# Kernel tuning notes

Measured on AMD Instinct MI355X. Metric: run time of the kernel, lower is better.

The kernel has to match this reference:

```python
import jax, jax.numpy as jnp
import numpy as np

LN_EPS = 1e-5


def setup_inputs() -> dict:
    key = jax.random.key(0)
    ks = jax.random.split(key, 6)
    B, I, H = 16384, 512, 512
    x = jax.random.normal(ks[0], (B, I), dtype=jnp.float32)
    h_prev = jax.random.normal(ks[1], (B, H), dtype=jnp.float32)
    c_prev = jax.random.normal(ks[2], (B, H), dtype=jnp.float32)
    # packed gate weights in i|f|g|o order (equivalent to 8 separate matmuls)
    W_i = jax.random.normal(ks[3], (I, 4 * H), dtype=jnp.float32) * (1.0 / np.sqrt(I))
    W_h = jax.random.normal(ks[4], (H, 4 * H), dtype=jnp.float32) * (1.0 / np.sqrt(H))
    # biases: b_i=0, b_f=1, b_g=0, b_o=0 as in the torch module
    b = jnp.concatenate([jnp.zeros(H), jnp.ones(H), jnp.zeros(H), jnp.zeros(H)]).astype(jnp.float32)
    ln_weight = jnp.ones((H,), dtype=jnp.float32)
    ln_bias = jnp.zeros((H,), dtype=jnp.float32)
    return {"x": x, "h_prev": h_prev, "c_prev": c_prev, "W_i": W_i, "W_h": W_h,
            "b": b, "ln_weight": ln_weight, "ln_bias": ln_bias}


def layer_norm(h, w, bias):
    mu = jnp.mean(h, axis=-1, keepdims=True)
    var = jnp.var(h, axis=-1, keepdims=True)
    return (h - mu) * jax.lax.rsqrt(var + LN_EPS) * w + bias


def reference(x, h_prev, c_prev, W_i, W_h, b, ln_weight, ln_bias):
    H = h_prev.shape[-1]
    # two fused GEMMs covering all 4 gates: [B, 4H]
    gates = x @ W_i + h_prev @ W_h + b
    i, f, g, o = jnp.split(gates, 4, axis=-1)
    i = jax.nn.sigmoid(i)
    f = jax.nn.sigmoid(f)
    g = jnp.tanh(g)
    o = jax.nn.sigmoid(o)
    c = f * c_prev + i * g
    h = o * jnp.tanh(c)
    h = layer_norm(h, ln_weight, ln_bias)
    return (h, c)
```

## Files before the change

### kernel.cpp

```cpp
#include <hip/hip_runtime.h>
#include <cstdint>
#include <cstddef>

typedef unsigned short ushort_t;
typedef __attribute__((ext_vector_type(8))) short bf16x8;
typedef __attribute__((ext_vector_type(4))) float f32x4;

#define MROWS 16384
#define KDIM  1024
#define NDIM  2048
#define HDIM  512

static __device__ __forceinline__ unsigned short f2bf(float f) {
    unsigned int u = __float_as_uint(f);
    u += 0x7fffu + ((u >> 16) & 1u);
    return (unsigned short)(u >> 16);
}

static __device__ __forceinline__ float sigmoid_f(float x) {
    return 1.0f / (1.0f + __expf(-x));
}
static __device__ __forceinline__ float tanh_f(float x) {
    float t = __expf(2.0f * x);
    return 1.0f - 2.0f / (t + 1.0f);
}

__global__ __launch_bounds__(256) void pack_ab(const float* __restrict__ x,
                                               const float* __restrict__ hp,
                                               const float* __restrict__ Wi,
                                               const float* __restrict__ Wh,
                                               ushort_t* __restrict__ A,
                                               ushort_t* __restrict__ Bt) {
    __shared__ ushort_t sm[64][72];
    const int tid = threadIdx.x;
    if (blockIdx.x < 8192) {
        int t = blockIdx.x * 256 + tid;
        int row = t >> 7;
        int kc = (t & 127) << 3;
        const float* src = (kc < 512) ? (x + (size_t)row * 512 + kc)
                                      : (hp + (size_t)row * 512 + (kc - 512));
        float4 v0 = ((const float4*)src)[0];
        float4 v1 = ((const float4*)src)[1];
        ushort_t o[8] __attribute__((aligned(16)));
        o[0] = f2bf(v0.x); o[1] = f2bf(v0.y); o[2] = f2bf(v0.z); o[3] = f2bf(v0.w);
        o[4] = f2bf(v1.x); o[5] = f2bf(v1.y); o[6] = f2bf(v1.z); o[7] = f2bf(v1.w);
        *((uint4*)(A + (size_t)row * KDIM + kc)) = *((const uint4*)o);
    } else {
        int b2 = blockIdx.x - 8192;
        int kt = b2 >> 5;
        int ct = b2 & 31;
        const float* W = (kt < 8) ? (Wi + (size_t)(kt * 64) * NDIM)
                                  : (Wh + (size_t)((kt - 8) * 64) * NDIM);
        int c0 = (tid & 15) * 4;
        int r0 = tid >> 4;
#pragma unroll
        for (int r = 0; r < 4; ++r) {
            int krow = r * 16 + r0;
            float4 v = *((const float4*)(W + (size_t)krow * NDIM + ct * 64 + c0));
            sm[krow][c0 + 0] = f2bf(v.x);
            sm[krow][c0 + 1] = f2bf(v.y);
            sm[krow][c0 + 2] = f2bf(v.z);
            sm[krow][c0 + 3] = f2bf(v.w);
        }
        __syncthreads();
        int g = (ct * 64) >> 9;
        int h0 = ct * 64 - g * 512;
#pragma unroll
        for (int q = tid; q < 512; q += 256) {
            int cc = q >> 3;
            int kc = (q & 7) * 8;
            ushort_t o[8] __attribute__((aligned(16)));
#pragma unroll
            for (int j = 0; j < 8; ++j) o[j] = sm[kc + j][cc];
            int np = 4 * (h0 + cc) + g;
            *((uint4*)(Bt + (size_t)np * KDIM + kt * 64 + kc)) = *((const uint4*)o);
        }
    }
}

__global__ __launch_bounds__(256, 4) void gemm_cell(const ushort_t* __restrict__ A,
                                                    const ushort_t* __restrict__ Bt,
                                                    const float* __restrict__ b,
                                                    const float* __restrict__ c_prev,
                                                    float* __restrict__ h_out,
                                                    float* __restrict__ c_out) {
    __shared__ float smem_f[10240];
    ushort_t* Als = (ushort_t*)smem_f;
    ushort_t* Bls = Als + 256 * 64;

    const int tid  = threadIdx.x;
    const int w    = tid >> 6;
    const int lane = tid & 63;
    int bid = blockIdx.x;
    int lid = (bid >> 3) + (bid & 7) * 256;
    const int m0 = (lid >> 5) * 256;
    const int n0 = (lid & 31) * 64;
    const int wm = w * 64;
    const int lr   = lane & 15;
    const int quad = lane >> 4;
    const int sw   = lr & 7;

    f32x4 zero = {0.f, 0.f, 0.f, 0.f};
    f32x4 acc[4][4];
#pragma unroll
    for (int i = 0; i < 4; ++i)
#pragma unroll
        for (int j = 0; j < 4; ++j) acc[i][j] = zero;

    for (int kt = 0; kt < KDIM / 64; ++kt) {
#pragma unroll
        for (int r = 0; r < 8; ++r) {
            int c = r * 256 + tid;
            int trow = c >> 3;
            int chg = (c & 7) ^ (trow & 7);
            const ushort_t* ga = A + (size_t)(m0 + trow) * KDIM + kt * 64 + chg * 8;
            __builtin_amdgcn_global_load_lds(
                (const __attribute__((address_space(1))) void*)ga,
                (__attribute__((address_space(3))) void*)((char*)Als + c * 16),
                16, 0, 0);
        }
#pragma unroll
        for (int r = 0; r < 2; ++r) {
            int c = r * 256 + tid;
            int trow = c >> 3;
            int chg = (c & 7) ^ (trow & 7);
            const ushort_t* gb = Bt + (size_t)(n0 + trow) * KDIM + kt * 64 + chg * 8;
            __builtin_amdgcn_global_load_lds(
                (const __attribute__((address_space(1))) void*)gb,
                (__attribute__((address_space(3))) void*)((char*)Bls + c * 16),
                16, 0, 0);
        }
        __syncthreads();

#pragma unroll
        for (int kk = 0; kk < 2; ++kk) {
            bf16x8 af[4], bfr[4];
            int ch = kk * 4 + quad;
#pragma unroll
            for (int t2 = 0; t2 < 4; ++t2) {
                int ra = wm + t2 * 16 + lr;
                af[t2] = *((const bf16x8*)(Als + (ra * 8 + (ch ^ sw)) * 8));
            }
#pragma unroll
            for (int t2 = 0; t2 < 4; ++t2) {
                int rb = t2 * 16 + lr;
                bfr[t2] = *((const bf16x8*)(Bls + (rb * 8 + (ch ^ sw)) * 8));
            }
#pragma unroll
            for (int tm = 0; tm < 4; ++tm)
#pragma unroll
                for (int tn = 0; tn < 4; ++tn)
                    acc[tm][tn] = __builtin_amdgcn_mfma_f32_16x16x32_bf16(
                        af[tm], bfr[tn], acc[tm][tn], 0, 0, 0);
        }
        __syncthreads();
    }

    float* scr = smem_f + w * 1024;
    const int rr = lane >> 2;
    const int hg0 = (n0 >> 2) + (lane & 3) * 4;
    const float4 bi4 = *((const float4*)(b + hg0));
    const float4 bff = *((const float4*)(b + 512 + hg0));
    const float4 bgg = *((const float4*)(b + 1024 + hg0));
    const float4 boo = *((const float4*)(b + 1536 + hg0));
    const float bi[4] = {bi4.x, bi4.y, bi4.z, bi4.w};
    const float bfv[4] = {bff.x, bff.y, bff.z, bff.w};
    const float bg[4] = {bgg.x, bgg.y, bgg.z, bgg.w};
    const float bo[4] = {boo.x, boo.y, boo.z, boo.w};

#pragma unroll
    for (int tm = 0; tm < 4; ++tm) {
#pragma unroll
        for (int tn = 0; tn < 4; ++tn) {
            int c = tn * 16 + lr;
#pragma unroll
            for (int rg = 0; rg < 4; ++rg) {
                int r = quad * 4 + rg;
                int blk = (c >> 2) ^ r;
                scr[r * 64 + blk * 4 + (c & 3)] = acc[tm][tn][rg];
            }
        }
        float4 gv[4];
#pragma unroll
        for (int j = 0; j < 4; ++j) {
            int cb = (lane & 3) * 4 + j;
            gv[j] = *((const float4*)(scr + rr * 64 + (cb ^ rr) * 4));
        }
        int grow = m0 + wm + tm * 16 + rr;
        float4 cp4 = *((const float4*)(c_prev + (size_t)grow * HDIM + hg0));
        const float cpv[4] = {cp4.x, cp4.y, cp4.z, cp4.w};
        float cn[4], hv[4];
#pragma unroll
        for (int j = 0; j < 4; ++j) {
            float iv = sigmoid_f(gv[j].x + bi[j]);
            float fv = sigmoid_f(gv[j].y + bfv[j]);
            float g2 = tanh_f(gv[j].z + bg[j]);
            float ov = sigmoid_f(gv[j].w + bo[j]);
            cn[j] = fv * cpv[j] + iv * g2;
            hv[j] = ov * tanh_f(cn[j]);
        }
        float4 cno = {cn[0], cn[1], cn[2], cn[3]};
        float4 hvo = {hv[0], hv[1], hv[2], hv[3]};
        *((float4*)(c_out + (size_t)grow * HDIM + hg0)) = cno;
        *((float4*)(h_out + (size_t)grow * HDIM + hg0)) = hvo;
    }
}

__global__ __launch_bounds__(256) void ln_kernel(float* __restrict__ h,
                                                 const float* __restrict__ lw,
                                                 const float* __restrict__ lb) {
    int w = threadIdx.x >> 6;
    int lane = threadIdx.x & 63;
    int row = blockIdx.x * 4 + w;
    float* p = h + (size_t)row * HDIM + lane * 8;
    float4 a = ((const float4*)p)[0];
    float4 c = ((const float4*)p)[1];
    float s  = a.x + a.y + a.z + a.w + c.x + c.y + c.z + c.w;
    float ss = a.x * a.x + a.y * a.y + a.z * a.z + a.w * a.w +
               c.x * c.x + c.y * c.y + c.z * c.z + c.w * c.w;
#pragma unroll
    for (int off = 32; off > 0; off >>= 1) {
        s  += __shfl_xor(s, off);
        ss += __shfl_xor(ss, off);
    }
    float mu = s * (1.0f / 512.0f);
    float var = ss * (1.0f / 512.0f) - mu * mu;
    float rstd = rsqrtf(var + 1e-5f);
    const float* wp = lw + lane * 8;
    const float* bp = lb + lane * 8;
    float4 w0 = ((const float4*)wp)[0];
    float4 w1 = ((const float4*)wp)[1];
    float4 b0 = ((const float4*)bp)[0];
    float4 b1 = ((const float4*)bp)[1];
    a.x = (a.x - mu) * rstd * w0.x + b0.x;
    a.y = (a.y - mu) * rstd * w0.y + b0.y;
    a.z = (a.z - mu) * rstd * w0.z + b0.z;
    a.w = (a.w - mu) * rstd * w0.w + b0.w;
    c.x = (c.x - mu) * rstd * w1.x + b1.x;
    c.y = (c.y - mu) * rstd * w1.y + b1.y;
    c.z = (c.z - mu) * rstd * w1.z + b1.z;
    c.w = (c.w - mu) * rstd * w1.w + b1.w;
    ((float4*)p)[0] = a;
    ((float4*)p)[1] = c;
}

extern "C" void kernel_launch(void* const* d_in, const int* in_sizes, int n_in,
                              void* d_out, int out_size, void* d_ws, size_t ws_size,
                              hipStream_t stream) {
    const float* x      = (const float*)d_in[0];
    const float* h_prev = (const float*)d_in[1];
    const float* c_prev = (const float*)d_in[2];
    const float* W_i    = (const float*)d_in[3];
    const float* W_h    = (const float*)d_in[4];
    const float* b      = (const float*)d_in[5];
    const float* ln_w   = (const float*)d_in[6];
    const float* ln_b   = (const float*)d_in[7];

    float* h_out = (float*)d_out;
    float* c_out = h_out + (size_t)MROWS * HDIM;

    ushort_t* A  = (ushort_t*)d_ws;
    ushort_t* Bt = A + (size_t)MROWS * KDIM;

    pack_ab<<<8192 + 512, 256, 0, stream>>>(x, h_prev, W_i, W_h, A, Bt);
    gemm_cell<<<2048, 256, 0, stream>>>(A, Bt, b, c_prev, h_out, c_out);
    ln_kernel<<<MROWS / 4, 256, 0, stream>>>(h_out, ln_w, ln_b);
}
```

Baseline: 254.8 us.

## Pre-pack A and B into MFMA fragment order and load directly to registers

The pack kernel now writes A and B in a tiled layout that matches the per-lane MFMA fragment order, 64x64 tiles with each lane's 8 bf16 contiguous. The GEMM then drops LDS staging and barriers and loads fragments straight from global memory into registers with coalesced 16-byte loads. This removes the LDS round trip and the __syncthreads. The cost is that each wave now fetches its own B tile instead of sharing it through LDS, and there is no software prefetch, so global latency is exposed inside the k-loop. Occupancy hints change from 4 to 3 blocks per CU.

```diff
diff --git a/kernel.cpp b/kernel.cpp
--- a/kernel.cpp
+++ b/kernel.cpp
@@ -24,81 +24,96 @@
     float t = __expf(2.0f * x);
     return 1.0f - 2.0f / (t + 1.0f);
 }
+
 
 __global__ __launch_bounds__(256) void pack_ab(const float* __restrict__ x,
                                                const float* __restrict__ hp,
                                                const float* __restrict__ Wi,
                                                const float* __restrict__ Wh,
                                                ushort_t* __restrict__ A,
-                                               ushort_t* __restrict__ Bt) {
+                                               ushort_t* __restrict__ B) {
     __shared__ ushort_t sm[64][72];
     const int tid = threadIdx.x;
-    if (blockIdx.x < 8192) {
-        int t = blockIdx.x * 256 + tid;
-        int row = t >> 7;
-        int kc = (t & 127) << 3;
-        const float* src = (kc < 512) ? (x + (size_t)row * 512 + kc)
-                                      : (hp + (size_t)row * 512 + (kc - 512));
+    if (blockIdx.x < 4096) {
+        int wt = blockIdx.x >> 4;
+        int kt = blockIdx.x & 15;
+        int r = tid >> 2;
+        int c0 = (tid & 3) * 16;
+        const float* src = (kt < 8)
+            ? (x  + (size_t)(wt * 64 + r) * 512 + kt * 64 + c0)
+            : (hp + (size_t)(wt * 64 + r) * 512 + (kt - 8) * 64 + c0);
         float4 v0 = ((const float4*)src)[0];
         float4 v1 = ((const float4*)src)[1];
-        ushort_t o[8] __attribute__((aligned(16)));
-        o[0] = f2bf(v0.x); o[1] = f2bf(v0.y); o[2] = f2bf(v0.z); o[3] = f2bf(v0.w);
-        o[4] = f2bf(v1.x); o[5] = f2bf(v1.y); o[6] = f2bf(v1.z); o[7] = f2bf(v1.w);
-        *((uint4*)(A + (size_t)row * KDIM + kc)) = *((const uint4*)o);
+        float4 v2 = ((const float4*)src)[2];
+        float4 v3 = ((const float4*)src)[3];
+        ushort_t* d = &sm[r][c0];
+        d[0]=f2bf(v0.x); d[1]=f2bf(v0.y); d[2]=f2bf(v0.z); d[3]=f2bf(v0.w);
+        d[4]=f2bf(v1.x); d[5]=f2bf(v1.y); d[6]=f2bf(v1.z); d[7]=f2bf(v1.w);
+        d[8]=f2bf(v2.x); d[9]=f2bf(v2.y); d[10]=f2bf(v2.z); d[11]=f2bf(v2.w);
+        d[12]=f2bf(v3.x); d[13]=f2bf(v3.y); d[14]=f2bf(v3.z); d[15]=f2bf(v3.w);
+        __syncthreads();
+        ushort_t* outb = A + (size_t)(wt * 16 + kt) * 4096;
+#pragma unroll
+        for (int i = 0; i < 2; ++i) {
+            int c = i * 256 + tid;
+            int lane = c & 63, t2 = (c >> 6) & 3, kk = c >> 8;
+            bf16x8 val = *((const bf16x8*)&sm[t2 * 16 + (lane & 15)]
+                                             [kk * 32 + (lane >> 4) * 8]);
+            *((bf16x8*)(outb + (size_t)c * 8)) = val;
+        }
     } else {
-        int b2 = blockIdx.x - 8192;
-        int kt = b2 >> 5;
-        int ct = b2 & 31;
-        const float* W = (kt < 8) ? (Wi + (size_t)(kt * 64) * NDIM)
-                                  : (Wh + (size_t)((kt - 8) * 64) * NDIM);
-        int c0 = (tid & 15) * 4;
-        int r0 = tid >> 4;
-#pragma unroll
-        for (int r = 0; r < 4; ++r) {
-            int krow = r * 16 + r0;
-            float4 v = *((const float4*)(W + (size_t)krow * NDIM + ct * 64 + c0));
-            sm[krow][c0 + 0] = f2bf(v.x);
-            sm[krow][c0 + 1] = f2bf(v.y);
-            sm[krow][c0 + 2] = f2bf(v.z);
-            sm[krow][c0 + 3] = f2bf(v.w);
-        }
+        int b2 = blockIdx.x - 4096;
+        int nt = b2 >> 4;
+        int kt = b2 & 15;
+        int r = tid >> 2;
+        int seg = tid & 3;
+        const float* Wsrc = (kt < 8)
+            ? (Wi + (size_t)(kt * 64 + r) * NDIM)
+            : (Wh + (size_t)((kt - 8) * 64 + r) * NDIM);
+        const float* p = Wsrc + seg * 512 + nt * 16;
+        float4 q0 = ((const float4*)p)[0];
+        float4 q1 = ((const float4*)p)[1];
+        float4 q2 = ((const float4*)p)[2];
+        float4 q3 = ((const float4*)p)[3];
+        float qv[16] = {q0.x,q0.y,q0.z,q0.w, q1.x,q1.y,q1.z,q1.w,
+                        q2.x,q2.y,q2.z,q2.w, q3.x,q3.y,q3.z,q3.w};
+#pragma unroll
+        for (int j = 0; j < 16; ++j)
+            sm[j * 4 + seg][r] = f2bf(qv[j]);
         __syncthreads();
-        int g = (ct * 64) >> 9;
-        int h0 = ct * 64 - g * 512;
-#pragma unroll
-        for (int q = tid; q < 512; q += 256) {
-            int cc = q >> 3;
-            int kc = (q & 7) * 8;
-            ushort_t o[8] __attribute__((aligned(16)));
-#pragma unroll
-            for (int j = 0; j < 8; ++j) o[j] = sm[kc + j][cc];
-            int np = 4 * (h0 + cc) + g;
-            *((uint4*)(Bt + (size_t)np * KDIM + kt * 64 + kc)) = *((const uint4*)o);
-        }
-    }
-}
-
-__global__ __launch_bounds__(256, 4) void gemm_cell(const ushort_t* __restrict__ A,
-                                                    const ushort_t* __restrict__ Bt,
+        ushort_t* outb = B + (size_t)(nt * 16 + kt) * 4096;
+#pragma unroll
+        for (int i = 0; i < 2; ++i) {
+            int c = i * 256 + tid;
+            int lane = c & 63, t2 = (c >> 6) & 3, kk = c >> 8;
+            bf16x8 val = *((const bf16x8*)&sm[t2 * 16 + (lane & 15)]
+                                             [kk * 32 + (lane >> 4) * 8]);
+            *((bf16x8*)(outb + (size_t)c * 8)) = val;
+        }
+    }
+}
+
+__global__ __launch_bounds__(256, 3) void gemm_cell(const ushort_t* __restrict__ A,
+                                                    const ushort_t* __restrict__ B,
                                                     const float* __restrict__ b,
                                                     const float* __restrict__ c_prev,
                                                     float* __restrict__ h_out,
                                                     float* __restrict__ c_out) {
-    __shared__ float smem_f[10240];
-    ushort_t* Als = (ushort_t*)smem_f;
-    ushort_t* Bls = Als + 256 * 64;
+    __shared__ float smem_f[4096];
 
     const int tid  = threadIdx.x;
     const int w    = tid >> 6;
     const int lane = tid & 63;
     int bid = blockIdx.x;
     int lid = (bid >> 3) + (bid & 7) * 256;
-    const int m0 = (lid >> 5) * 256;
-    const int n0 = (lid & 31) * 64;
-    const int wm = w * 64;
+    const int mb = lid >> 5;
+    const int nt = lid & 31;
+    const int wt = mb * 4 + w;
     const int lr   = lane & 15;
     const int quad = lane >> 4;
-    const int sw   = lr & 7;
+
+    const ushort_t* Abase = A + (size_t)wt * 16 * 4096 + lane * 8;
+    const ushort_t* Bbase = B + (size_t)nt * 16 * 4096 + lane * 8;
 
     f32x4 zero = {0.f, 0.f, 0.f, 0.f};
     f32x4 acc[4][4];
@@ -107,58 +122,31 @@
 #pragma unroll
         for (int j = 0; j < 4; ++j) acc[i][j] = zero;
 
-    for (int kt = 0; kt < KDIM / 64; ++kt) {
-#pragma unroll
-        for (int r = 0; r < 8; ++r) {
-            int c = r * 256 + tid;
-            int trow = c >> 3;
-            int chg = (c & 7) ^ (trow & 7);
-            const ushort_t* ga = A + (size_t)(m0 + trow) * KDIM + kt * 64 + chg * 8;
-            __builtin_amdgcn_global_load_lds(
-                (const __attribute__((address_space(1))) void*)ga,
-                (__attribute__((address_space(3))) void*)((char*)Als + c * 16),
-                16, 0, 0);
-        }
-#pragma unroll
-        for (int r = 0; r < 2; ++r) {
-            int c = r * 256 + tid;
-            int trow = c >> 3;
-            int chg = (c & 7) ^ (trow & 7);
-            const ushort_t* gb = Bt + (size_t)(n0 + trow) * KDIM + kt * 64 + chg * 8;
-            __builtin_amdgcn_global_load_lds(
-                (const __attribute__((address_space(1))) void*)gb,
-                (__attribute__((address_space(3))) void*)((char*)Bls + c * 16),
-                16, 0, 0);
-        }
-        __syncthreads();
-
-#pragma unroll
-        for (int kk = 0; kk < 2; ++kk) {
-            bf16x8 af[4], bfr[4];
-            int ch = kk * 4 + quad;
+#pragma unroll 1
+    for (int kt = 0; kt < 16; ++kt) {
+        const ushort_t* pa = Abase + kt * 4096;
+        const ushort_t* pb = Bbase + kt * 4096;
+        bf16x8 af[2][4], bf[2][4];
+#pragma unroll
+        for (int kk = 0; kk < 2; ++kk)
 #pragma unroll
             for (int t2 = 0; t2 < 4; ++t2) {
-                int ra = wm + t2 * 16 + lr;
-                af[t2] = *((const bf16x8*)(Als + (ra * 8 + (ch ^ sw)) * 8));
+                af[kk][t2] = *((const bf16x8*)(pa + (kk * 4 + t2) * 512));
+                bf[kk][t2] = *((const bf16x8*)(pb + (kk * 4 + t2) * 512));
             }
 #pragma unroll
-            for (int t2 = 0; t2 < 4; ++t2) {
-                int rb = t2 * 16 + lr;
-                bfr[t2] = *((const bf16x8*)(Bls + (rb * 8 + (ch ^ sw)) * 8));
-            }
+        for (int kk = 0; kk < 2; ++kk)
 #pragma unroll
             for (int tm = 0; tm < 4; ++tm)
 #pragma unroll
                 for (int tn = 0; tn < 4; ++tn)
                     acc[tm][tn] = __builtin_amdgcn_mfma_f32_16x16x32_bf16(
-                        af[tm], bfr[tn], acc[tm][tn], 0, 0, 0);
-        }
-        __syncthreads();
+                        af[kk][tm], bf[kk][tn], acc[tm][tn], 0, 0, 0);
     }
 
     float* scr = smem_f + w * 1024;
     const int rr = lane >> 2;
-    const int hg0 = (n0 >> 2) + (lane & 3) * 4;
+    const int hg0 = nt * 16 + (lane & 3) * 4;
     const float4 bi4 = *((const float4*)(b + hg0));
     const float4 bff = *((const float4*)(b + 512 + hg0));
     const float4 bgg = *((const float4*)(b + 1024 + hg0));
@@ -186,7 +174,7 @@
             int cb = (lane & 3) * 4 + j;
             gv[j] = *((const float4*)(scr + rr * 64 + (cb ^ rr) * 4));
         }
-        int grow = m0 + wm + tm * 16 + rr;
+        int grow = wt * 64 + tm * 16 + rr;
         float4 cp4 = *((const float4*)(c_prev + (size_t)grow * HDIM + hg0));
         const float cpv[4] = {cp4.x, cp4.y, cp4.z, cp4.w};
         float cn[4], hv[4];
@@ -260,9 +248,9 @@
     float* c_out = h_out + (size_t)MROWS * HDIM;
 
     ushort_t* A  = (ushort_t*)d_ws;
-    ushort_t* Bt = A + (size_t)MROWS * KDIM;
-
-    pack_ab<<<8192 + 512, 256, 0, stream>>>(x, h_prev, W_i, W_h, A, Bt);
-    gemm_cell<<<2048, 256, 0, stream>>>(A, Bt, b, c_prev, h_out, c_out);
+    ushort_t* B  = A + (size_t)MROWS * KDIM;
+
+    pack_ab<<<4096 + 512, 256, 0, stream>>>(x, h_prev, W_i, W_h, A, B);
+    gemm_cell<<<2048, 256, 0, stream>>>(A, B, b, c_prev, h_out, c_out);
     ln_kernel<<<MROWS / 4, 256, 0, stream>>>(h_out, ln_w, ln_b);
 }
```

New measurement: 259.0 us. Within noise of the previous version (+1.6%).
